# Kernel optimization log

Hardware: AMD Instinct MI355X
Metric: run time of the kernel (lower is better)

The kernel has to match this reference:

```python
import jax, jax.numpy as jnp
import numpy as np


def setup_inputs() -> dict:
    key = jax.random.key(0)
    ks = jax.random.split(key, 5)
    n, raw, d, h = 1024, 128, 128, 256
    s = lambda fan: 1.0 / np.sqrt(fan)
    return {
        "x": jax.random.normal(ks[0], (n, raw), jnp.float32),
        "W_enc": jax.random.normal(ks[1], (raw, d), jnp.float32) * s(raw),
        "b_enc": jnp.zeros((d,), jnp.float32),
        "W1": jax.random.normal(ks[2], (2 * d, h), jnp.float32) * s(2 * d),
        "b1": jnp.zeros((h,), jnp.float32),
        "W2": jax.random.normal(ks[3], (h, 1), jnp.float32) * s(h),
        "b2": jnp.zeros((1,), jnp.float32),
    }


def reference(x, W_enc, b_enc, W1, b1, W2, b2):
    # pathVAE.encode stand-in: linear projection to latent mean
    z = x @ W_enc + b_enc                      # [n, d]
    n, d = z.shape
    # Original builds feat[i, j] = concat(z[j], z[i]) of shape [n*n, 2d],
    # then Linear(2d->h). Split W1 so the quadratic concat is never built:
    # h[i, j] = z[j] @ W1[:d] + z[i] @ W1[d:] + b1
    A = z @ W1[:d]                             # acts on the "a" (j) half
    B = z @ W1[d:]                             # acts on the "b" (i) half
    hmat = A[None, :, :] + B[:, None, :] + b1  # [n, n, h]
    hmat = jax.nn.selu(hmat)
    o = hmat @ W2 + b2                         # [n, n, 1]
    o = jax.nn.hard_sigmoid(o)                 # relu6(x+3)/6, same as torch
    return o.reshape(n, n)
```

## Files before the change

kernel.cpp:

```cpp
#include <hip/hip_runtime.h>
#include <math.h>


#define LOG2E       1.4426950408889634f
#define SELU_AS     1.7580993408473766f
#define S_OVER_L2E  0.7282921587620419f
#define INV64       0.015625f

typedef float v2f __attribute__((ext_vector_type(2)));
typedef _Float16 v2h __attribute__((ext_vector_type(2)));
typedef unsigned int u32;

__global__ __launch_bounds__(256) void prep_kernel(
    const float* __restrict__ x, const float* __restrict__ W_enc,
    const float* __restrict__ b_enc, const float* __restrict__ W1,
    const float* __restrict__ b1, const float* __restrict__ W2,
    const float* __restrict__ b2, u32* __restrict__ PAa,
    u32* __restrict__ PAe, u32* __restrict__ PBb, u32* __restrict__ PBe,
    u32* __restrict__ W2m, u32* __restrict__ W2e, float* __restrict__ basep)
{
    __shared__ float zs[512];
    int t = threadIdx.x, b = blockIdx.x;
    if (b < 256) {
        int r0 = b << 2;
        int r = t >> 6;
        int dd = (t & 63) << 1;
        const float* xr = x + (size_t)(r0 + r) * 128;
        v2f z = { b_enc[dd], b_enc[dd + 1] };
#pragma unroll 8
        for (int dl = 0; dl < 128; ++dl) {
            float xv = xr[dl];
            v2f xx = { xv, xv };
            v2f wv = *(const v2f*)(W_enc + (size_t)dl * 128 + dd);
            z = __builtin_elementwise_fma(xx, wv, z);
        }
        zs[r * 128 + dd] = z.x;
        zs[r * 128 + dd + 1] = z.y;
        __syncthreads();

        int c = t;
        float b1c = b1[c];
        float accA0 = 0.f, accA1 = 0.f, accA2 = 0.f, accA3 = 0.f;
        float accB0 = b1c, accB1 = b1c, accB2 = b1c, accB3 = b1c;
        const float* w1a = W1 + c;
        const float* w1b = W1 + 128 * 256 + c;
#pragma unroll 4
        for (int dl = 0; dl < 128; ++dl) {
            float wa = w1a[(size_t)dl * 256];
            float wb = w1b[(size_t)dl * 256];
            float z0 = zs[dl], z1 = zs[128 + dl], z2 = zs[256 + dl], z3 = zs[384 + dl];
            accA0 = fmaf(z0, wa, accA0); accB0 = fmaf(z0, wb, accB0);
            accA1 = fmaf(z1, wa, accA1); accB1 = fmaf(z1, wb, accB1);
            accA2 = fmaf(z2, wa, accA2); accB2 = fmaf(z2, wb, accB2);
            accA3 = fmaf(z3, wa, accA3); accB3 = fmaf(z3, wb, accB3);
        }
        float ar[4] = { accA0 * LOG2E, accA1 * LOG2E, accA2 * LOG2E, accA3 * LOG2E };
        float br[4] = { accB0 * LOG2E, accB1 * LOG2E, accB2 * LOG2E, accB3 * LOG2E };
        u32 pa[4], pe[4], pb[4], pf[4];
        bool odd = (c & 1);
#pragma unroll
        for (int r2 = 0; r2 < 4; ++r2) {
            float er = __builtin_amdgcn_exp2f(ar[r2]);
            float fr = __builtin_amdgcn_exp2f(br[r2]);
            float aN = __shfl_xor(ar[r2], 1);
            float eN = __shfl_xor(er, 1);
            float bN = __shfl_xor(br[r2], 1);
            float fN = __shfl_xor(fr, 1);
            pa[r2] = __builtin_bit_cast(u32,
                __builtin_amdgcn_cvt_pkrtz(ar[r2] * INV64, aN * INV64));
            pe[r2] = __builtin_bit_cast(u32, __builtin_amdgcn_cvt_pkrtz(er, eN));
            pb[r2] = __builtin_bit_cast(u32,
                __builtin_amdgcn_cvt_pkrtz(bN * INV64, br[r2] * INV64));
            pf[r2] = __builtin_bit_cast(u32, __builtin_amdgcn_cvt_pkrtz(fN, fr));
        }
        size_t o = (size_t)(c >> 1) * 1024 + r0;
        if (!odd) {
            *(uint4*)(PAa + o) = make_uint4(pa[0], pa[1], pa[2], pa[3]);
            *(uint4*)(PAe + o) = make_uint4(pe[0], pe[1], pe[2], pe[3]);
        } else {
            *(uint4*)(PBb + o) = make_uint4(pb[0], pb[1], pb[2], pb[3]);
            *(uint4*)(PBe + o) = make_uint4(pf[0], pf[1], pf[2], pf[3]);
        }
    } else {
        if (t < 128) {
            float w0 = W2[2 * t], w1 = W2[2 * t + 1];
            const float S64 = S_OVER_L2E * 64.0f;
            W2m[t] = __builtin_bit_cast(u32,
                __builtin_amdgcn_cvt_pkrtz(S64 * w0, S64 * w1));
            W2e[t] = __builtin_bit_cast(u32,
                __builtin_amdgcn_cvt_pkrtz(SELU_AS * w0, SELU_AS * w1));
        }
        if (t < 64) {
            float s = W2[t] + W2[t + 64] + W2[t + 128] + W2[t + 192];
#pragma unroll
            for (int o = 32; o > 0; o >>= 1) s += __shfl_down(s, o);
            if (t == 0) basep[0] = fmaf(-SELU_AS, s, b2[0]);
        }
    }
}

__device__ __forceinline__ v2h clamp2(v2h v) {
    const v2h z = { (_Float16)0.f, (_Float16)0.f };
    const v2h o = { (_Float16)1.f, (_Float16)1.f };
    return __builtin_elementwise_min(__builtin_elementwise_max(v, z), o);
}

__global__ __launch_bounds__(512, 2) void pair_kernel(
    const u32* __restrict__ PAa, const u32* __restrict__ PAe,
    const u32* __restrict__ PBb, const u32* __restrict__ PBe,
    const u32* __restrict__ W2m, const u32* __restrict__ W2e,
    const float* __restrict__ basep, float* __restrict__ out)
{
    __shared__ __align__(16) u32 S[16384];

    int t = threadIdx.x;
    int w = t >> 6;
    int lt = t & 63;
    int bj64 = blockIdx.x << 6, bi64 = blockIdx.y << 6;
    int jb = (lt & 7) << 3;
    int ib = (lt >> 3) << 3;

    u32* Q  = S + (w << 11);
    u32* Aa = Q;
    u32* Ae = Q + 512;
    u32* Bb = Q + 1024;
    u32* Be = Q + 1536;

    float acc[8][8];
#pragma unroll
    for (int i = 0; i < 8; ++i)
#pragma unroll
        for (int j = 0; j < 8; ++j) acc[i][j] = 0.f;

    for (int sc = 0; sc < 2; ++sc) {
        int k2base = (w << 4) + (sc << 3);
        asm volatile("" ::: "memory");
#pragma unroll
        for (int p = 0; p < 2; ++p) {
            int idx = (p << 6) + lt;
            int row = idx >> 4;
            int col = (idx & 15) << 2;
            size_t go = (size_t)(k2base + row) * 1024;
            *(uint4*)&Aa[idx << 2] = *(const uint4*)(PAa + go + bj64 + col);
            *(uint4*)&Ae[idx << 2] = *(const uint4*)(PAe + go + bj64 + col);
            *(uint4*)&Bb[idx << 2] = *(const uint4*)(PBb + go + bi64 + col);
            *(uint4*)&Be[idx << 2] = *(const uint4*)(PBe + go + bi64 + col);
        }
        asm volatile("s_waitcnt lgkmcnt(0)" ::: "memory");

        const u32* Wm = W2m + k2base;
        const u32* We = W2e + k2base;
#pragma unroll 4
        for (int k2 = 0; k2 < 8; ++k2) {
            v2h w2m = __builtin_bit_cast(v2h, Wm[k2]);
            v2h w2e = __builtin_bit_cast(v2h, We[k2]);
            uint4 qa0 = *(const uint4*)&Aa[(k2 << 6) + jb];
            uint4 qa1 = *(const uint4*)&Aa[(k2 << 6) + jb + 4];
            uint4 qe0 = *(const uint4*)&Ae[(k2 << 6) + jb];
            uint4 qe1 = *(const uint4*)&Ae[(k2 << 6) + jb + 4];
            uint4 qb0 = *(const uint4*)&Bb[(k2 << 6) + ib];
            uint4 qb1 = *(const uint4*)&Bb[(k2 << 6) + ib + 4];
            uint4 qf0 = *(const uint4*)&Be[(k2 << 6) + ib];
            uint4 qf1 = *(const uint4*)&Be[(k2 << 6) + ib + 4];
            v2h A[8] = { __builtin_bit_cast(v2h, qa0.x), __builtin_bit_cast(v2h, qa0.y),
                         __builtin_bit_cast(v2h, qa0.z), __builtin_bit_cast(v2h, qa0.w),
                         __builtin_bit_cast(v2h, qa1.x), __builtin_bit_cast(v2h, qa1.y),
                         __builtin_bit_cast(v2h, qa1.z), __builtin_bit_cast(v2h, qa1.w) };
            v2h E[8] = { __builtin_bit_cast(v2h, qe0.x), __builtin_bit_cast(v2h, qe0.y),
                         __builtin_bit_cast(v2h, qe0.z), __builtin_bit_cast(v2h, qe0.w),
                         __builtin_bit_cast(v2h, qe1.x), __builtin_bit_cast(v2h, qe1.y),
                         __builtin_bit_cast(v2h, qe1.z), __builtin_bit_cast(v2h, qe1.w) };
            v2h B[8] = { __builtin_bit_cast(v2h, qb0.x), __builtin_bit_cast(v2h, qb0.y),
                         __builtin_bit_cast(v2h, qb0.z), __builtin_bit_cast(v2h, qb0.w),
                         __builtin_bit_cast(v2h, qb1.x), __builtin_bit_cast(v2h, qb1.y),
                         __builtin_bit_cast(v2h, qb1.z), __builtin_bit_cast(v2h, qb1.w) };
            v2h F[8] = { __builtin_bit_cast(v2h, qf0.x), __builtin_bit_cast(v2h, qf0.y),
                         __builtin_bit_cast(v2h, qf0.z), __builtin_bit_cast(v2h, qf0.w),
                         __builtin_bit_cast(v2h, qf1.x), __builtin_bit_cast(v2h, qf1.y),
                         __builtin_bit_cast(v2h, qf1.z), __builtin_bit_cast(v2h, qf1.w) };
#pragma unroll
            for (int i = 0; i < 8; ++i) {
#pragma unroll
                for (int j = 0; j < 8; ++j) {
                    v2h t2 = clamp2(A[j] + B[i]);
                    v2h p2 = clamp2(E[j] * F[i]);
                    acc[i][j] = __builtin_amdgcn_fdot2(t2, w2m, acc[i][j], false);
                    acc[i][j] = __builtin_amdgcn_fdot2(p2, w2e, acc[i][j], false);
                }
            }
        }
    }

    float4* buf = (float4*)S;
#define STORE_ACC(REG) {                                                  \
        float4* r_ = buf + ((REG) << 10);                                 \
        _Pragma("unroll")                                                 \
        for (int i = 0; i < 8; ++i) {                                     \
            float4 lo = { acc[i][0], acc[i][1], acc[i][2], acc[i][3] };   \
            float4 hi = { acc[i][4], acc[i][5], acc[i][6], acc[i][7] };   \
            r_[((i << 1) + 0) * 64 + lt] = lo;                            \
            r_[((i << 1) + 1) * 64 + lt] = hi;                            \
        } }
#define ADD_ACC(REG) {                                                    \
        float4* r_ = buf + ((REG) << 10);                                 \
        _Pragma("unroll")                                                 \
        for (int i = 0; i < 8; ++i) {                                     \
            float4 lo = r_[((i << 1) + 0) * 64 + lt];                     \
            float4 hi = r_[((i << 1) + 1) * 64 + lt];                     \
            acc[i][0] += lo.x; acc[i][1] += lo.y;                         \
            acc[i][2] += lo.z; acc[i][3] += lo.w;                         \
            acc[i][4] += hi.x; acc[i][5] += hi.y;                         \
            acc[i][6] += hi.z; acc[i][7] += hi.w;                         \
        } }

    __syncthreads();
    if (w >= 4) STORE_ACC(w - 4);
    __syncthreads();
    if (w < 4) ADD_ACC(w);
    __syncthreads();
    if (w == 2 || w == 3) STORE_ACC(w - 2);
    __syncthreads();
    if (w < 2) ADD_ACC(w);
    __syncthreads();
    if (w == 1) STORE_ACC(0);
    __syncthreads();
    if (w == 0) {
        ADD_ACC(0);
        float base = basep[0];
#pragma unroll
        for (int i = 0; i < 8; ++i) {
            float4 o0, o1;
            o0.x = __saturatef((acc[i][0] + base) * (1.0f / 6.0f) + 0.5f);
            o0.y = __saturatef((acc[i][1] + base) * (1.0f / 6.0f) + 0.5f);
            o0.z = __saturatef((acc[i][2] + base) * (1.0f / 6.0f) + 0.5f);
            o0.w = __saturatef((acc[i][3] + base) * (1.0f / 6.0f) + 0.5f);
            o1.x = __saturatef((acc[i][4] + base) * (1.0f / 6.0f) + 0.5f);
            o1.y = __saturatef((acc[i][5] + base) * (1.0f / 6.0f) + 0.5f);
            o1.z = __saturatef((acc[i][6] + base) * (1.0f / 6.0f) + 0.5f);
            o1.w = __saturatef((acc[i][7] + base) * (1.0f / 6.0f) + 0.5f);
            size_t orow = (size_t)(bi64 + ib + i) * 1024 + bj64 + jb;
            *(float4*)(out + orow) = o0;
            *(float4*)(out + orow + 4) = o1;
        }
    }
#undef STORE_ACC
#undef ADD_ACC
}

extern "C" void kernel_launch(void* const* d_in, const int* in_sizes, int n_in,
                              void* d_out, int out_size, void* d_ws, size_t ws_size,
                              hipStream_t stream) {
    const float* x     = (const float*)d_in[0];
    const float* W_enc = (const float*)d_in[1];
    const float* b_enc = (const float*)d_in[2];
    const float* W1    = (const float*)d_in[3];
    const float* b1    = (const float*)d_in[4];
    const float* W2    = (const float*)d_in[5];
    const float* b2    = (const float*)d_in[6];
    float* out = (float*)d_out;

    u32* ws = (u32*)d_ws;
    const int PLANE = 128 * 1024;
    u32* PAa = ws;
    u32* PAe = ws + PLANE;
    u32* PBb = ws + 2 * PLANE;
    u32* PBe = ws + 3 * PLANE;
    u32* W2m = ws + 4 * PLANE;
    u32* W2e = ws + 4 * PLANE + 128;
    float* basep = (float*)(ws + 4 * PLANE + 256);

    prep_kernel<<<257, 256, 0, stream>>>(x, W_enc, b_enc, W1, b1, W2, b2,
                                         PAa, PAe, PBb, PBe, W2m, W2e, basep);
    pair_kernel<<<dim3(16, 16), 512, 0, stream>>>(PAa, PAe, PBb, PBe,
                                                  W2m, W2e, basep, out);
}
```

Baseline: 104.1 us.

## Halve pair-kernel i-tile to 32 rows and raise occupancy to four blocks

The pair kernel's output tile shrinks from 64x64 to 32x64, so each thread holds a 4x8 accumulator instead of 8x8, and the grid doubles to 16x32 blocks. Launch bounds move to 4 blocks per CU and shared memory drops to 48KB to allow the extra residency. The W2 weights are now preloaded into registers with vector loads and the k2 loop is fully unrolled. The smaller tile lowers register pressure and fills more of the CU. In exchange, each A/E element loaded is reused across fewer rows, so the A planes are read more times in total.

```diff
diff --git a/kernel.cpp b/kernel.cpp
--- a/kernel.cpp
+++ b/kernel.cpp
@@ -105,30 +105,31 @@
     return __builtin_elementwise_min(__builtin_elementwise_max(v, z), o);
 }
 
-__global__ __launch_bounds__(512, 2) void pair_kernel(
+__global__ __launch_bounds__(512, 4) void pair_kernel(
     const u32* __restrict__ PAa, const u32* __restrict__ PAe,
     const u32* __restrict__ PBb, const u32* __restrict__ PBe,
     const u32* __restrict__ W2m, const u32* __restrict__ W2e,
     const float* __restrict__ basep, float* __restrict__ out)
 {
-    __shared__ __align__(16) u32 S[16384];
+    __shared__ __align__(16) u32 S[12288];
 
     int t = threadIdx.x;
     int w = t >> 6;
     int lt = t & 63;
-    int bj64 = blockIdx.x << 6, bi64 = blockIdx.y << 6;
+    int bj64 = blockIdx.x << 6;
+    int bi32 = blockIdx.y << 5;
     int jb = (lt & 7) << 3;
-    int ib = (lt >> 3) << 3;
-
-    u32* Q  = S + (w << 11);
+    int ib = (lt >> 3) << 2;
+
+    u32* Q  = S + w * 1536;
     u32* Aa = Q;
     u32* Ae = Q + 512;
     u32* Bb = Q + 1024;
-    u32* Be = Q + 1536;
-
-    float acc[8][8];
-#pragma unroll
-    for (int i = 0; i < 8; ++i)
+    u32* Be = Q + 1280;
+
+    float acc[4][8];
+#pragma unroll
+    for (int i = 0; i < 4; ++i)
 #pragma unroll
         for (int j = 0; j < 8; ++j) acc[i][j] = 0.f;
 
@@ -143,25 +144,32 @@
             size_t go = (size_t)(k2base + row) * 1024;
             *(uint4*)&Aa[idx << 2] = *(const uint4*)(PAa + go + bj64 + col);
             *(uint4*)&Ae[idx << 2] = *(const uint4*)(PAe + go + bj64 + col);
-            *(uint4*)&Bb[idx << 2] = *(const uint4*)(PBb + go + bi64 + col);
-            *(uint4*)&Be[idx << 2] = *(const uint4*)(PBe + go + bi64 + col);
-        }
+        }
+        {
+            int row = lt >> 3;
+            int col = (lt & 7) << 2;
+            size_t go = (size_t)(k2base + row) * 1024;
+            *(uint4*)&Bb[lt << 2] = *(const uint4*)(PBb + go + bi32 + col);
+            *(uint4*)&Be[lt << 2] = *(const uint4*)(PBe + go + bi32 + col);
+        }
+        uint4 wm0 = *(const uint4*)(W2m + k2base);
+        uint4 wm1 = *(const uint4*)(W2m + k2base + 4);
+        uint4 we0 = *(const uint4*)(W2e + k2base);
+        uint4 we1 = *(const uint4*)(W2e + k2base + 4);
+        u32 wmv[8] = { wm0.x, wm0.y, wm0.z, wm0.w, wm1.x, wm1.y, wm1.z, wm1.w };
+        u32 wev[8] = { we0.x, we0.y, we0.z, we0.w, we1.x, we1.y, we1.z, we1.w };
         asm volatile("s_waitcnt lgkmcnt(0)" ::: "memory");
 
-        const u32* Wm = W2m + k2base;
-        const u32* We = W2e + k2base;
-#pragma unroll 4
+#pragma unroll
         for (int k2 = 0; k2 < 8; ++k2) {
-            v2h w2m = __builtin_bit_cast(v2h, Wm[k2]);
-            v2h w2e = __builtin_bit_cast(v2h, We[k2]);
+            v2h w2m = __builtin_bit_cast(v2h, wmv[k2]);
+            v2h w2e = __builtin_bit_cast(v2h, wev[k2]);
             uint4 qa0 = *(const uint4*)&Aa[(k2 << 6) + jb];
             uint4 qa1 = *(const uint4*)&Aa[(k2 << 6) + jb + 4];
             uint4 qe0 = *(const uint4*)&Ae[(k2 << 6) + jb];
             uint4 qe1 = *(const uint4*)&Ae[(k2 << 6) + jb + 4];
-            uint4 qb0 = *(const uint4*)&Bb[(k2 << 6) + ib];
-            uint4 qb1 = *(const uint4*)&Bb[(k2 << 6) + ib + 4];
-            uint4 qf0 = *(const uint4*)&Be[(k2 << 6) + ib];
-            uint4 qf1 = *(const uint4*)&Be[(k2 << 6) + ib + 4];
+            uint4 qb  = *(const uint4*)&Bb[(k2 << 5) + ib];
+            uint4 qf  = *(const uint4*)&Be[(k2 << 5) + ib];
             v2h A[8] = { __builtin_bit_cast(v2h, qa0.x), __builtin_bit_cast(v2h, qa0.y),
                          __builtin_bit_cast(v2h, qa0.z), __builtin_bit_cast(v2h, qa0.w),
                          __builtin_bit_cast(v2h, qa1.x), __builtin_bit_cast(v2h, qa1.y),
@@ -170,20 +178,16 @@
                          __builtin_bit_cast(v2h, qe0.z), __builtin_bit_cast(v2h, qe0.w),
                          __builtin_bit_cast(v2h, qe1.x), __builtin_bit_cast(v2h, qe1.y),
                          __builtin_bit_cast(v2h, qe1.z), __builtin_bit_cast(v2h, qe1.w) };
-            v2h B[8] = { __builtin_bit_cast(v2h, qb0.x), __builtin_bit_cast(v2h, qb0.y),
-                         __builtin_bit_cast(v2h, qb0.z), __builtin_bit_cast(v2h, qb0.w),
-                         __builtin_bit_cast(v2h, qb1.x), __builtin_bit_cast(v2h, qb1.y),
-                         __builtin_bit_cast(v2h, qb1.z), __builtin_bit_cast(v2h, qb1.w) };
-            v2h F[8] = { __builtin_bit_cast(v2h, qf0.x), __builtin_bit_cast(v2h, qf0.y),
-                         __builtin_bit_cast(v2h, qf0.z), __builtin_bit_cast(v2h, qf0.w),
-                         __builtin_bit_cast(v2h, qf1.x), __builtin_bit_cast(v2h, qf1.y),
-                         __builtin_bit_cast(v2h, qf1.z), __builtin_bit_cast(v2h, qf1.w) };
-#pragma unroll
-            for (int i = 0; i < 8; ++i) {
+            v2h B4[4] = { __builtin_bit_cast(v2h, qb.x), __builtin_bit_cast(v2h, qb.y),
+                          __builtin_bit_cast(v2h, qb.z), __builtin_bit_cast(v2h, qb.w) };
+            v2h F4[4] = { __builtin_bit_cast(v2h, qf.x), __builtin_bit_cast(v2h, qf.y),
+                          __builtin_bit_cast(v2h, qf.z), __builtin_bit_cast(v2h, qf.w) };
+#pragma unroll
+            for (int i = 0; i < 4; ++i) {
 #pragma unroll
                 for (int j = 0; j < 8; ++j) {
-                    v2h t2 = clamp2(A[j] + B[i]);
-                    v2h p2 = clamp2(E[j] * F[i]);
+                    v2h t2 = clamp2(A[j] + B4[i]);
+                    v2h p2 = clamp2(E[j] * F4[i]);
                     acc[i][j] = __builtin_amdgcn_fdot2(t2, w2m, acc[i][j], false);
                     acc[i][j] = __builtin_amdgcn_fdot2(p2, w2e, acc[i][j], false);
                 }
@@ -193,18 +197,18 @@
 
     float4* buf = (float4*)S;
 #define STORE_ACC(REG) {                                                  \
-        float4* r_ = buf + ((REG) << 10);                                 \
+        float4* r_ = buf + ((REG) * 512);                                 \
         _Pragma("unroll")                                                 \
-        for (int i = 0; i < 8; ++i) {                                     \
+        for (int i = 0; i < 4; ++i) {                                     \
             float4 lo = { acc[i][0], acc[i][1], acc[i][2], acc[i][3] };   \
             float4 hi = { acc[i][4], acc[i][5], acc[i][6], acc[i][7] };   \
             r_[((i << 1) + 0) * 64 + lt] = lo;                            \
             r_[((i << 1) + 1) * 64 + lt] = hi;                            \
         } }
 #define ADD_ACC(REG) {                                                    \
-        float4* r_ = buf + ((REG) << 10);                                 \
+        float4* r_ = buf + ((REG) * 512);                                 \
         _Pragma("unroll")                                                 \
-        for (int i = 0; i < 8; ++i) {                                     \
+        for (int i = 0; i < 4; ++i) {                                     \
             float4 lo = r_[((i << 1) + 0) * 64 + lt];                     \
             float4 hi = r_[((i << 1) + 1) * 64 + lt];                     \
             acc[i][0] += lo.x; acc[i][1] += lo.y;                         \
@@ -228,7 +232,7 @@
         ADD_ACC(0);
         float base = basep[0];
 #pragma unroll
-        for (int i = 0; i < 8; ++i) {
+        for (int i = 0; i < 4; ++i) {
             float4 o0, o1;
             o0.x = __saturatef((acc[i][0] + base) * (1.0f / 6.0f) + 0.5f);
             o0.y = __saturatef((acc[i][1] + base) * (1.0f / 6.0f) + 0.5f);
@@ -238,7 +242,7 @@
             o1.y = __saturatef((acc[i][5] + base) * (1.0f / 6.0f) + 0.5f);
             o1.z = __saturatef((acc[i][6] + base) * (1.0f / 6.0f) + 0.5f);
             o1.w = __saturatef((acc[i][7] + base) * (1.0f / 6.0f) + 0.5f);
-            size_t orow = (size_t)(bi64 + ib + i) * 1024 + bj64 + jb;
+            size_t orow = (size_t)(bi32 + ib + i) * 1024 + bj64 + jb;
             *(float4*)(out + orow) = o0;
             *(float4*)(out + orow + 4) = o1;
         }
@@ -271,6 +275,6 @@
 
     prep_kernel<<<257, 256, 0, stream>>>(x, W_enc, b_enc, W1, b1, W2, b2,
                                          PAa, PAe, PBb, PBe, W2m, W2e, basep);
-    pair_kernel<<<dim3(16, 16), 512, 0, stream>>>(PAa, PAe, PBb, PBe,
+    pair_kernel<<<dim3(16, 32), 512, 0, stream>>>(PAa, PAe, PBb, PBe,
                                                   W2m, W2e, basep, out);
 }
```

Result: no change. 105.6 us (+1.4%).

## Prefetch second k-chunk into registers and remap blocks for XCD locality

Applied to the files above, without the earlier changes.

Global loads for the second k-chunk are now issued into registers while the first chunk is computed, so load latency overlaps with math instead of sitting between chunks. The grid also becomes 1-D with a swizzled block-to-tile mapping that groups blocks sharing the same B rows onto the same XCD, aiming for better L2 reuse. The cost is more live registers for the prefetch buffers, which could pressure occupancy under launch_bounds(512,2). An unused hone constant is also added.

```diff
diff --git a/kernel.cpp b/kernel.cpp
--- a/kernel.cpp
+++ b/kernel.cpp
@@ -116,7 +116,11 @@
     int t = threadIdx.x;
     int w = t >> 6;
     int lt = t & 63;
-    int bj64 = blockIdx.x << 6, bi64 = blockIdx.y << 6;
+    int b = blockIdx.x;
+    int x8 = b & 7, q = b >> 3;
+    int bi_idx = (x8 << 1) + (q >> 4);
+    int bj_idx = q & 15;
+    int bj64 = bj_idx << 6, bi64 = bi_idx << 6;
     int jb = (lt & 7) << 3;
     int ib = (lt >> 3) << 3;
 
@@ -132,19 +136,50 @@
 #pragma unroll
         for (int j = 0; j < 8; ++j) acc[i][j] = 0.f;
 
+    const v2h hone = { (_Float16)1.f, (_Float16)1.f };
+
+    int s_row[2], s_col[2];
+#pragma unroll
+    for (int p = 0; p < 2; ++p) {
+        int idx = (p << 6) + lt;
+        s_row[p] = idx >> 4;
+        s_col[p] = (idx & 15) << 2;
+    }
+
+    uint4 ga[2], ge[2], gb[2], gf[2];
+    {
+        int k2base = (w << 4);
+#pragma unroll
+        for (int p = 0; p < 2; ++p) {
+            size_t go = (size_t)(k2base + s_row[p]) * 1024;
+            ga[p] = *(const uint4*)(PAa + go + bj64 + s_col[p]);
+            ge[p] = *(const uint4*)(PAe + go + bj64 + s_col[p]);
+            gb[p] = *(const uint4*)(PBb + go + bi64 + s_col[p]);
+            gf[p] = *(const uint4*)(PBe + go + bi64 + s_col[p]);
+        }
+    }
+
     for (int sc = 0; sc < 2; ++sc) {
         int k2base = (w << 4) + (sc << 3);
         asm volatile("" ::: "memory");
 #pragma unroll
         for (int p = 0; p < 2; ++p) {
             int idx = (p << 6) + lt;
-            int row = idx >> 4;
-            int col = (idx & 15) << 2;
-            size_t go = (size_t)(k2base + row) * 1024;
-            *(uint4*)&Aa[idx << 2] = *(const uint4*)(PAa + go + bj64 + col);
-            *(uint4*)&Ae[idx << 2] = *(const uint4*)(PAe + go + bj64 + col);
-            *(uint4*)&Bb[idx << 2] = *(const uint4*)(PBb + go + bi64 + col);
-            *(uint4*)&Be[idx << 2] = *(const uint4*)(PBe + go + bi64 + col);
+            *(uint4*)&Aa[idx << 2] = ga[p];
+            *(uint4*)&Ae[idx << 2] = ge[p];
+            *(uint4*)&Bb[idx << 2] = gb[p];
+            *(uint4*)&Be[idx << 2] = gf[p];
+        }
+        if (sc == 0) {
+            int k2n = (w << 4) + 8;
+#pragma unroll
+            for (int p = 0; p < 2; ++p) {
+                size_t go = (size_t)(k2n + s_row[p]) * 1024;
+                ga[p] = *(const uint4*)(PAa + go + bj64 + s_col[p]);
+                ge[p] = *(const uint4*)(PAe + go + bj64 + s_col[p]);
+                gb[p] = *(const uint4*)(PBb + go + bi64 + s_col[p]);
+                gf[p] = *(const uint4*)(PBe + go + bi64 + s_col[p]);
+            }
         }
         asm volatile("s_waitcnt lgkmcnt(0)" ::: "memory");
 
@@ -271,6 +306,6 @@
 
     prep_kernel<<<257, 256, 0, stream>>>(x, W_enc, b_enc, W1, b1, W2, b2,
                                          PAa, PAe, PBb, PBe, W2m, W2e, basep);
-    pair_kernel<<<dim3(16, 16), 512, 0, stream>>>(PAa, PAe, PBb, PBe,
-                                                  W2m, W2e, basep, out);
+    pair_kernel<<<256, 512, 0, stream>>>(PAa, PAe, PBb, PBe,
+                                         W2m, W2e, basep, out);
 }
```

After: 136.3 us. 30.9% more time.
